# Kernel tuning notes

Hardware: AMD Instinct MI355X
Metric: run time of the kernel (lower is better)

The kernel has to match this reference:

```python
import jax, jax.numpy as jnp
import numpy as np

LEN = 8388608  # 2**23, must be a power of 2


def setup_inputs() -> dict:
    key = jax.random.key(0)
    k1, k2 = jax.random.split(key)
    inp = jax.random.normal(k1, (LEN,), dtype=jnp.float32)
    weight = jax.random.uniform(k2, (LEN // 2, 2), dtype=jnp.float32)  # learned twiddle factors
    return {"input": inp, "weight": weight}


def _complex_mul(a, w):
    # a: [d, cols, 2] complex pairs; w: [cols, 2] broadcast over leading dim
    ar, ai = a[:, :, 0], a[:, :, 1]
    wr, wi = w[:, 0], w[:, 1]
    return jnp.stack([ar * wr - ai * wi, ar * wi + ai * wr], axis=-1)


def reference(input, weight):
    n = input.shape[0]
    # real signal -> complex pairs, shape [n, 1, 2]
    x = jnp.stack([input, jnp.zeros_like(input)], axis=-1)[:, None, :]
    d = n // 2
    while d != 0:  # log2(n) static stages
        w = weight[0::d]          # [cols, 2] where cols == x.shape[1]
        top = x[:d]               # [d, cols, 2]
        bot = x[d:]               # [d, cols, 2]
        p = _complex_mul(bot, w)  # butterfly twiddle multiply
        x = jnp.concatenate([top + p, top - p], axis=1)  # [d, 2*cols, 2]
        d //= 2
    return x  # [1, n, 2]
```

## Files before the change

### kernel.cpp

```cpp
#include <hip/hip_runtime.h>
#include <hip/hip_fp16.h>

__device__ __forceinline__ float2 cadd(float2 a, float2 b) { return make_float2(a.x + b.x, a.y + b.y); }
__device__ __forceinline__ float2 csub(float2 a, float2 b) { return make_float2(a.x - b.x, a.y - b.y); }
__device__ __forceinline__ float2 cmul(float2 w, float2 z) {
    return make_float2(w.x * z.x - w.y * z.y, w.x * z.y + w.y * z.x);
}
__device__ __forceinline__ unsigned pk(float2 z) {
    __half2 h = __floats2half2_rn(z.x, z.y);
    return *reinterpret_cast<unsigned*>(&h);
}
__device__ __forceinline__ float2 upk(unsigned u) {
    __half2 h = *reinterpret_cast<__half2*>(&u);
    return __half22float2(h);
}

__host__ __device__ constexpr unsigned crev(unsigned x, int bits) {
    unsigned r = 0;
    for (int k = 0; k < bits; ++k) r |= ((x >> k) & 1u) << (bits - 1 - k);
    return r;
}


__global__ __launch_bounds__(256) void fft_pass_a(const float* __restrict__ in,
                                                  const float2* __restrict__ wt,
                                                  uint4* __restrict__ outp)
{
    __shared__ float2 L[4096];
    const int tid = threadIdx.x;
    const int l0  = blockIdx.x << 4;
    const int c   = tid & 15;
    const int qb  = tid >> 4;

    float2 pw1[4], pw2a[4], pw2b[4];
#pragma unroll
    for (int k = 0; k < 4; ++k) { pw1[k] = wt[0]; pw2a[k] = wt[0]; pw2b[k] = wt[1 << 21]; }

    {
        const int c4 = tid & 3, gg = tid >> 2;
#pragma unroll
        for (int k = 0; k < 4; ++k) {
            const int g = gg + (k << 6);
            const float4 v = *reinterpret_cast<const float4*>(in + ((size_t)g << 15) + l0 + (c4 << 2));
            const int base = (g << 4) + (c4 << 2);
            L[base + 0] = make_float2(v.x, 0.f);
            L[base + 1] = make_float2(v.y, 0.f);
            L[base + 2] = make_float2(v.z, 0.f);
            L[base + 3] = make_float2(v.w, 0.f);
        }
    }
    __syncthreads();

#pragma unroll
    for (int rho = 0; rho < 4; ++rho) {
        const int s = rho << 1, H = 128 >> s, Q = H >> 1, lo = 6 - s;
        float2 nw1[4], nw2a[4], nw2b[4];
        if (rho < 3) {
            const int s2 = s + 2, lo2 = 6 - s2;
#pragma unroll
            for (int k = 0; k < 4; ++k) {
                const int qi = (qb << 2) + k;
                const int b  = ((qi >> lo2) << (lo2 + 2)) | (qi & ((1 << lo2) - 1));
                const int jl = (int)(__brev((unsigned)(b >> (8 - s2))) >> (32 - s2));
                const int e  = jl << (21 - s2);
                nw1[k] = wt[e << 1]; nw2a[k] = wt[e]; nw2b[k] = wt[e + (1 << 21)];
            }
        }
#pragma unroll
        for (int k = 0; k < 4; ++k) {
            const int qi = (qb << 2) + k;
            const int b  = ((qi >> lo) << (lo + 2)) | (qi & ((1 << lo) - 1));
            const int iA = (b << 4) + c;
            const float2 A  = L[iA];
            const float2 Bv = L[iA + (Q << 4)];
            const float2 Cv = L[iA + (H << 4)];
            const float2 Dv = L[iA + ((H + Q) << 4)];
            const float2 pC = cmul(pw1[k], Cv), pD = cmul(pw1[k], Dv);
            const float2 tA = cadd(A, pC),  tC = csub(A, pC);
            const float2 tB = cadd(Bv, pD), tD = csub(Bv, pD);
            const float2 p2 = cmul(pw2a[k], tB);
            const float2 p3 = cmul(pw2b[k], tD);
            L[iA]                  = cadd(tA, p2);
            L[iA + (Q << 4)]       = csub(tA, p2);
            L[iA + (H << 4)]       = cadd(tC, p3);
            L[iA + ((H + Q) << 4)] = csub(tC, p3);
        }
        __syncthreads();
        if (rho < 3) {
#pragma unroll
            for (int k = 0; k < 4; ++k) { pw1[k] = nw1[k]; pw2a[k] = nw2a[k]; pw2b[k] = nw2b[k]; }
        }
    }

    {
        const int c4 = tid & 3, gg = tid >> 2;
#pragma unroll
        for (int k = 0; k < 4; ++k) {
            const int g  = gg + (k << 6);
            const int li = (g << 4) + (c4 << 2);
            uint4 v;
            v.x = pk(L[li]); v.y = pk(L[li + 1]); v.z = pk(L[li + 2]); v.w = pk(L[li + 3]);
            outp[((size_t)g << 13) + (l0 >> 2) + c4] = v;
        }
    }
}

__global__ __launch_bounds__(256) void fft_pass_b(const unsigned* __restrict__ in,
                                                  const float2* __restrict__ wt,
                                                  unsigned* __restrict__ out)
{
    const int tid = threadIdx.x;
    const int h   = blockIdx.x >> 2;
    const int low = ((blockIdx.x & 3) << 8) | tid;
    const unsigned hrev = __brev((unsigned)h) >> 24;
    const unsigned base = ((unsigned)h << 15) | (unsigned)low;

    float2 X[32];
#pragma unroll
    for (int m = 0; m < 32; ++m) X[m] = upk(in[base + ((unsigned)m << 10)]);

#pragma unroll
    for (int s = 0; s < 5; ++s) {
        const int half = 1 << (4 - s);
#pragma unroll
        for (int j = 0; j < 16; ++j) {
            const int mh = j >> (4 - s);
            const int lo = (mh << (5 - s)) | (j & (half - 1));
            const int hi = lo | half;
            const unsigned cr = crev((unsigned)mh, s);
            const float2 w = wt[(((cr << 8) | hrev) << (14 - s))];
            const float2 p = cmul(w, X[hi]);
            X[hi] = csub(X[lo], p);
            X[lo] = cadd(X[lo], p);
        }
    }
#pragma unroll
    for (int m = 0; m < 32; ++m) out[base + ((unsigned)m << 10)] = pk(X[m]);
}

__global__ __launch_bounds__(512, 4) void fft_pass_c(const uint4* __restrict__ inp4,
                                                     const float2* __restrict__ wt,
                                                     float2* __restrict__ out)
{
    extern __shared__ float2 L[];
    const int tid = threadIdx.x;
    const int h0  = blockIdx.x;
    const int lam = tid & 7;
    const int bq  = tid >> 3;
    const int R   = (h0 << 3) | lam;

    {
        const int f  = tid & 63;
        const int lm = tid >> 6;
        const unsigned H = __brev((unsigned)((h0 << 3) | lm)) >> 19;
        const size_t gb = ((size_t)H << 8);
#pragma unroll
        for (int k = 0; k < 4; ++k) {
            const uint4 v = inp4[gb + (k << 6) + f];
            const int base = lm * 1026 + (k << 8) + (f << 2);
            const float2 e0 = upk(v.x), e1 = upk(v.y), e2 = upk(v.z), e3 = upk(v.w);
            *reinterpret_cast<float4*>(&L[base])     = make_float4(e0.x, e0.y, e1.x, e1.y);
            *reinterpret_cast<float4*>(&L[base + 2]) = make_float4(e2.x, e2.y, e3.x, e3.y);
        }
    }
    __syncthreads();

#pragma unroll
    for (int rho = 0; rho < 4; ++rho) {
        const int sh = 8 - (rho << 1);
        const int Q  = 1 << sh;
        const int H2 = Q << 1;
#pragma unroll
        for (int k = 0; k < 4; ++k) {
            const int qi = (k << 6) | bq;
            const int x  = ((qi >> sh) << (sh + 2)) | (qi & (Q - 1));
            const int a  = x >> (sh + 2);
            const unsigned xr = rho ? (__brev((unsigned)a) >> (32 - (rho << 1))) : 0u;
            const int e  = (int)((((xr << 13) | (unsigned)R)) << sh);
            const float2 w1  = wt[e << 1];
            const float2 w2a = wt[e];
            const float2 w2b = wt[e + (1 << 21)];
            const int iA = lam * 1026 + x;
            const float2 A  = L[iA];
            const float2 Bv = L[iA + Q];
            const float2 Cv = L[iA + H2];
            const float2 Dv = L[iA + H2 + Q];
            const float2 pC = cmul(w1, Cv), pD = cmul(w1, Dv);
            const float2 tA = cadd(A, pC),  tC = csub(A, pC);
            const float2 tB = cadd(Bv, pD), tD = csub(Bv, pD);
            const float2 p2 = cmul(w2a, tB);
            const float2 p3 = cmul(w2b, tD);
            L[iA]           = cadd(tA, p2);
            L[iA + Q]       = csub(tA, p2);
            L[iA + H2]      = cadd(tC, p3);
            L[iA + H2 + Q]  = csub(tC, p3);
        }
        __syncthreads();
    }

    {
#pragma unroll
        for (int k = 0; k < 4; ++k) {
            const int qi = (k << 6) | bq;
            const int x  = qi << 2;
            const unsigned xr = __brev((unsigned)qi) >> 24;
            const int e  = (int)((xr << 13) | (unsigned)R);
            const float2 w1  = wt[e << 1];
            const float2 w2a = wt[e];
            const float2 w2b = wt[e + (1 << 21)];
            const int iA = lam * 1026 + x;
            const float4 f0 = *reinterpret_cast<const float4*>(&L[iA]);
            const float4 f1 = *reinterpret_cast<const float4*>(&L[iA + 2]);
            const float2 A  = make_float2(f0.x, f0.y);
            const float2 Bv = make_float2(f0.z, f0.w);
            const float2 Cv = make_float2(f1.x, f1.y);
            const float2 Dv = make_float2(f1.z, f1.w);
            const float2 pC = cmul(w1, Cv), pD = cmul(w1, Dv);
            const float2 tA = cadd(A, pC),  tC = csub(A, pC);
            const float2 tB = cadd(Bv, pD), tD = csub(Bv, pD);
            const float2 p2 = cmul(w2a, tB);
            const float2 p3 = cmul(w2b, tD);
            const float2 rA = cadd(tA, p2), rB = csub(tA, p2);
            const float2 rC = cadd(tC, p3), rD = csub(tC, p3);
            *reinterpret_cast<float4*>(&L[iA])     = make_float4(rA.x, rA.y, rB.x, rB.y);
            *reinterpret_cast<float4*>(&L[iA + 2]) = make_float4(rC.x, rC.y, rD.x, rD.y);
        }
    }
    __syncthreads();

    {
        const int l2 = (tid & 3) << 1;
        const int xb = tid >> 2;
#pragma unroll
        for (int k = 0; k < 8; ++k) {
            const int x = (k << 7) | xb;
            const float2 a0 = L[l2 * 1026 + x];
            const float2 a1 = L[(l2 + 1) * 1026 + x];
            const size_t o = ((size_t)(__brev((unsigned)x) >> 22) << 13)
                           | (unsigned)((h0 << 3) | l2);
            *reinterpret_cast<float4*>(out + o) = make_float4(a0.x, a0.y, a1.x, a1.y);
        }
    }
}

extern "C" void kernel_launch(void* const* d_in, const int* in_sizes, int n_in,
                              void* d_out, int out_size, void* d_ws, size_t ws_size,
                              hipStream_t stream)
{
    (void)in_sizes; (void)n_in; (void)out_size; (void)ws_size;
    const float*  in = (const float*)d_in[0];
    const float2* wt = (const float2*)d_in[1];
    float2* outc = (float2*)d_out;
    uint4*  buf1 = (uint4*)d_ws;
    unsigned* buf2 = (unsigned*)((char*)d_ws + (32u << 20));

    static bool attr_done = false;
    if (!attr_done) {
        (void)hipFuncSetAttribute(reinterpret_cast<const void*>(fft_pass_c),
                                  hipFuncAttributeMaxDynamicSharedMemorySize, 8 * 1026 * 8);
        attr_done = true;
    }

    fft_pass_a<<<2048, 256, 0, stream>>>(in, wt, buf1);
    fft_pass_b<<<1024, 256, 0, stream>>>((const unsigned*)buf1, wt, buf2);
    fft_pass_c<<<1024, 512, 8 * 1026 * 8, stream>>>((const uint4*)buf2, wt, outc);
}
```

Before: 198.4 us.

## Use nontemporal loads/stores, widen pass C blocks, prefetch twiddles, swizzle block order

Global loads and stores in all three passes become nontemporal so streaming data does not pollute the caches. Pass C now runs 1024 threads per block, with two butterflies per thread instead of four. Its twiddles are prefetched into registers one stage ahead so their latency overlaps the LDS work, and the block index is permuted to change which blocks run together. This trades more registers and higher occupancy pressure for better latency hiding, and the nontemporal hints could hurt if data would have been reused in L2.

Result: no change. 201.7 us (+1.7%).

```diff
diff --git a/kernel.cpp b/kernel.cpp
--- a/kernel.cpp
+++ b/kernel.cpp
@@ -1,5 +1,8 @@
 #include <hip/hip_runtime.h>
 #include <hip/hip_fp16.h>
+
+typedef float    f4 __attribute__((ext_vector_type(4)));
+typedef unsigned u4 __attribute__((ext_vector_type(4)));
 
 __device__ __forceinline__ float2 cadd(float2 a, float2 b) { return make_float2(a.x + b.x, a.y + b.y); }
 __device__ __forceinline__ float2 csub(float2 a, float2 b) { return make_float2(a.x - b.x, a.y - b.y); }
@@ -41,12 +44,13 @@
 #pragma unroll
         for (int k = 0; k < 4; ++k) {
             const int g = gg + (k << 6);
-            const float4 v = *reinterpret_cast<const float4*>(in + ((size_t)g << 15) + l0 + (c4 << 2));
+            const f4 v = __builtin_nontemporal_load(
+                reinterpret_cast<const f4*>(in + ((size_t)g << 15) + l0 + (c4 << 2)));
             const int base = (g << 4) + (c4 << 2);
-            L[base + 0] = make_float2(v.x, 0.f);
-            L[base + 1] = make_float2(v.y, 0.f);
-            L[base + 2] = make_float2(v.z, 0.f);
-            L[base + 3] = make_float2(v.w, 0.f);
+            L[base + 0] = make_float2(v[0], 0.f);
+            L[base + 1] = make_float2(v[1], 0.f);
+            L[base + 2] = make_float2(v[2], 0.f);
+            L[base + 3] = make_float2(v[3], 0.f);
         }
     }
     __syncthreads();
@@ -98,9 +102,10 @@
         for (int k = 0; k < 4; ++k) {
             const int g  = gg + (k << 6);
             const int li = (g << 4) + (c4 << 2);
-            uint4 v;
-            v.x = pk(L[li]); v.y = pk(L[li + 1]); v.z = pk(L[li + 2]); v.w = pk(L[li + 3]);
-            outp[((size_t)g << 13) + (l0 >> 2) + c4] = v;
+            u4 v;
+            v[0] = pk(L[li]); v[1] = pk(L[li + 1]); v[2] = pk(L[li + 2]); v[3] = pk(L[li + 3]);
+            __builtin_nontemporal_store(v,
+                reinterpret_cast<u4*>(&outp[((size_t)g << 13) + (l0 >> 2) + c4]));
         }
     }
 }
@@ -117,7 +122,8 @@
 
     float2 X[32];
 #pragma unroll
-    for (int m = 0; m < 32; ++m) X[m] = upk(in[base + ((unsigned)m << 10)]);
+    for (int m = 0; m < 32; ++m)
+        X[m] = upk(__builtin_nontemporal_load(&in[base + ((unsigned)m << 10)]));
 
 #pragma unroll
     for (int s = 0; s < 5; ++s) {
@@ -135,34 +141,47 @@
         }
     }
 #pragma unroll
-    for (int m = 0; m < 32; ++m) out[base + ((unsigned)m << 10)] = pk(X[m]);
-}
-
-__global__ __launch_bounds__(512, 4) void fft_pass_c(const uint4* __restrict__ inp4,
-                                                     const float2* __restrict__ wt,
-                                                     float2* __restrict__ out)
+    for (int m = 0; m < 32; ++m)
+        __builtin_nontemporal_store(pk(X[m]), &out[base + ((unsigned)m << 10)]);
+}
+
+__global__ __launch_bounds__(1024, 8) void fft_pass_c(const uint4* __restrict__ inp4,
+                                                      const float2* __restrict__ wt,
+                                                      float2* __restrict__ out)
 {
     extern __shared__ float2 L[];
     const int tid = threadIdx.x;
-    const int h0  = blockIdx.x;
+    const int bid = blockIdx.x;
+    const int h0  = ((bid & 7) << 7) | (bid >> 3);
     const int lam = tid & 7;
     const int bq  = tid >> 3;
     const int R   = (h0 << 3) | lam;
 
     {
-        const int f  = tid & 63;
-        const int lm = tid >> 6;
+        const int f    = tid & 63;
+        const int lm   = (tid >> 6) & 7;
+        const int half = tid >> 9;
         const unsigned H = __brev((unsigned)((h0 << 3) | lm)) >> 19;
         const size_t gb = ((size_t)H << 8);
 #pragma unroll
-        for (int k = 0; k < 4; ++k) {
-            const uint4 v = inp4[gb + (k << 6) + f];
-            const int base = lm * 1026 + (k << 8) + (f << 2);
-            const float2 e0 = upk(v.x), e1 = upk(v.y), e2 = upk(v.z), e3 = upk(v.w);
+        for (int k = 0; k < 2; ++k) {
+            const int slot = (half << 7) | (k << 6) | f;
+            const u4 v = __builtin_nontemporal_load(
+                reinterpret_cast<const u4*>(&inp4[gb + slot]));
+            const int base = lm * 1026 + (slot << 2);
+            const float2 e0 = upk(v[0]), e1 = upk(v[1]), e2 = upk(v[2]), e3 = upk(v[3]);
             *reinterpret_cast<float4*>(&L[base])     = make_float4(e0.x, e0.y, e1.x, e1.y);
             *reinterpret_cast<float4*>(&L[base + 2]) = make_float4(e2.x, e2.y, e3.x, e3.y);
         }
     }
+
+    float2 w1[2], w2a[2], w2b[2];
+#pragma unroll
+    for (int k = 0; k < 2; ++k) {
+        const int e = R << 8;
+        w1[k] = wt[e << 1]; w2a[k] = wt[e]; w2b[k] = wt[e + (1 << 21)];
+    }
+    float2 f1[2], f2a[2], f2b[2];
     __syncthreads();
 
 #pragma unroll
@@ -170,56 +189,69 @@
         const int sh = 8 - (rho << 1);
         const int Q  = 1 << sh;
         const int H2 = Q << 1;
-#pragma unroll
-        for (int k = 0; k < 4; ++k) {
-            const int qi = (k << 6) | bq;
+        float2 nw1[2], nw2a[2], nw2b[2];
+        if (rho < 3) {
+            const int rn = rho + 1, shn = 8 - (rn << 1);
+#pragma unroll
+            for (int k = 0; k < 2; ++k) {
+                const int qi = (k << 7) | bq;
+                const unsigned ar = (unsigned)(qi >> shn);
+                const unsigned xr = __brev(ar) >> (32 - (rn << 1));
+                const int e = (int)(((xr << 13) | (unsigned)R) << shn);
+                nw1[k] = wt[e << 1]; nw2a[k] = wt[e]; nw2b[k] = wt[e + (1 << 21)];
+            }
+        } else {
+#pragma unroll
+            for (int k = 0; k < 2; ++k) {
+                const int qi = (k << 7) | bq;
+                const unsigned xr = __brev((unsigned)qi) >> 24;
+                const int e = (int)((xr << 13) | (unsigned)R);
+                f1[k] = wt[e << 1]; f2a[k] = wt[e]; f2b[k] = wt[e + (1 << 21)];
+            }
+        }
+#pragma unroll
+        for (int k = 0; k < 2; ++k) {
+            const int qi = (k << 7) | bq;
             const int x  = ((qi >> sh) << (sh + 2)) | (qi & (Q - 1));
-            const int a  = x >> (sh + 2);
-            const unsigned xr = rho ? (__brev((unsigned)a) >> (32 - (rho << 1))) : 0u;
-            const int e  = (int)((((xr << 13) | (unsigned)R)) << sh);
-            const float2 w1  = wt[e << 1];
-            const float2 w2a = wt[e];
-            const float2 w2b = wt[e + (1 << 21)];
             const int iA = lam * 1026 + x;
             const float2 A  = L[iA];
             const float2 Bv = L[iA + Q];
             const float2 Cv = L[iA + H2];
             const float2 Dv = L[iA + H2 + Q];
-            const float2 pC = cmul(w1, Cv), pD = cmul(w1, Dv);
+            const float2 pC = cmul(w1[k], Cv), pD = cmul(w1[k], Dv);
             const float2 tA = cadd(A, pC),  tC = csub(A, pC);
             const float2 tB = cadd(Bv, pD), tD = csub(Bv, pD);
-            const float2 p2 = cmul(w2a, tB);
-            const float2 p3 = cmul(w2b, tD);
+            const float2 p2 = cmul(w2a[k], tB);
+            const float2 p3 = cmul(w2b[k], tD);
             L[iA]           = cadd(tA, p2);
             L[iA + Q]       = csub(tA, p2);
             L[iA + H2]      = cadd(tC, p3);
             L[iA + H2 + Q]  = csub(tC, p3);
         }
         __syncthreads();
-    }
-
-    {
-#pragma unroll
-        for (int k = 0; k < 4; ++k) {
-            const int qi = (k << 6) | bq;
+        if (rho < 3) {
+#pragma unroll
+            for (int k = 0; k < 2; ++k) { w1[k] = nw1[k]; w2a[k] = nw2a[k]; w2b[k] = nw2b[k]; }
+        }
+    }
+
+    {
+#pragma unroll
+        for (int k = 0; k < 2; ++k) {
+            const int qi = (k << 7) | bq;
             const int x  = qi << 2;
-            const unsigned xr = __brev((unsigned)qi) >> 24;
-            const int e  = (int)((xr << 13) | (unsigned)R);
-            const float2 w1  = wt[e << 1];
-            const float2 w2a = wt[e];
-            const float2 w2b = wt[e + (1 << 21)];
             const int iA = lam * 1026 + x;
-            const float4 f0 = *reinterpret_cast<const float4*>(&L[iA]);
-            const float4 f1 = *reinterpret_cast<const float4*>(&L[iA + 2]);
-            const float2 A  = make_float2(f0.x, f0.y);
-            const float2 Bv = make_float2(f0.z, f0.w);
-            const float2 Cv = make_float2(f1.x, f1.y);
-            const float2 Dv = make_float2(f1.z, f1.w);
-            const float2 pC = cmul(w1, Cv), pD = cmul(w1, Dv);
+            const float4 g0 = *reinterpret_cast<const float4*>(&L[iA]);
+            const float4 g1 = *reinterpret_cast<const float4*>(&L[iA + 2]);
+            const float2 A  = make_float2(g0.x, g0.y);
+            const float2 Bv = make_float2(g0.z, g0.w);
+            const float2 Cv = make_float2(g1.x, g1.y);
+            const float2 Dv = make_float2(g1.z, g1.w);
+            const float2 pC = cmul(f1[k], Cv), pD = cmul(f1[k], Dv);
             const float2 tA = cadd(A, pC),  tC = csub(A, pC);
             const float2 tB = cadd(Bv, pD), tD = csub(Bv, pD);
-            const float2 p2 = cmul(w2a, tB);
-            const float2 p3 = cmul(w2b, tD);
+            const float2 p2 = cmul(f2a[k], tB);
+            const float2 p3 = cmul(f2b[k], tD);
             const float2 rA = cadd(tA, p2), rB = csub(tA, p2);
             const float2 rC = cadd(tC, p3), rD = csub(tC, p3);
             *reinterpret_cast<float4*>(&L[iA])     = make_float4(rA.x, rA.y, rB.x, rB.y);
@@ -229,16 +261,17 @@
     __syncthreads();
 
     {
-        const int l2 = (tid & 3) << 1;
-        const int xb = tid >> 2;
-#pragma unroll
-        for (int k = 0; k < 8; ++k) {
-            const int x = (k << 7) | xb;
+        const int l2   = (tid & 3) << 1;
+        const int rest = tid >> 2;
+#pragma unroll
+        for (int k = 0; k < 4; ++k) {
+            const int x = (k << 8) | rest;
             const float2 a0 = L[l2 * 1026 + x];
             const float2 a1 = L[(l2 + 1) * 1026 + x];
             const size_t o = ((size_t)(__brev((unsigned)x) >> 22) << 13)
                            | (unsigned)((h0 << 3) | l2);
-            *reinterpret_cast<float4*>(out + o) = make_float4(a0.x, a0.y, a1.x, a1.y);
+            f4 sv; sv[0] = a0.x; sv[1] = a0.y; sv[2] = a1.x; sv[3] = a1.y;
+            __builtin_nontemporal_store(sv, reinterpret_cast<f4*>(out + o));
         }
     }
 }
@@ -263,5 +296,5 @@
 
     fft_pass_a<<<2048, 256, 0, stream>>>(in, wt, buf1);
     fft_pass_b<<<1024, 256, 0, stream>>>((const unsigned*)buf1, wt, buf2);
-    fft_pass_c<<<1024, 512, 8 * 1026 * 8, stream>>>((const uint4*)buf2, wt, outc);
-}
+    fft_pass_c<<<1024, 1024, 8 * 1026 * 8, stream>>>((const uint4*)buf2, wt, outc);
+}
```

## Merge three FFT passes into two kernels with 12+11 stage split

Applied to the files above, without the earlier changes.

Restructures the 23-stage FFT from three global-memory passes into two. The first kernel does 12 stages per column set using registers and a padded shared-memory transpose, and the second does the remaining 11 stages in shared memory. This removes one full round trip of the fp16 intermediate buffer through global memory. In exchange it uses larger blocks (1024 threads), more shared memory per block, and more register pressure, so occupancy may drop.

New measurement: 226.0 us. 1.14x slower.

```diff
diff --git a/kernel.cpp b/kernel.cpp
--- a/kernel.cpp
+++ b/kernel.cpp
@@ -14,6 +14,11 @@
     __half2 h = *reinterpret_cast<__half2*>(&u);
     return __half22float2(h);
 }
+__device__ __forceinline__ void bf(float2& lo, float2& hi, float2 w) {
+    const float2 p = cmul(w, hi);
+    hi = csub(lo, p);
+    lo = cadd(lo, p);
+}
 
 __host__ __device__ constexpr unsigned crev(unsigned x, int bits) {
     unsigned r = 0;
@@ -22,103 +27,24 @@
 }
 
 
-__global__ __launch_bounds__(256) void fft_pass_a(const float* __restrict__ in,
+__global__ __launch_bounds__(1024) void fft_pass1(const float* __restrict__ in,
                                                   const float2* __restrict__ wt,
-                                                  uint4* __restrict__ outp)
+                                                  unsigned* __restrict__ outp)
 {
-    __shared__ float2 L[4096];
-    const int tid = threadIdx.x;
-    const int l0  = blockIdx.x << 4;
-    const int c   = tid & 15;
-    const int qb  = tid >> 4;
-
-    float2 pw1[4], pw2a[4], pw2b[4];
-#pragma unroll
-    for (int k = 0; k < 4; ++k) { pw1[k] = wt[0]; pw2a[k] = wt[0]; pw2b[k] = wt[1 << 21]; }
-
+    extern __shared__ unsigned LD[];
+    const int tid  = threadIdx.x;
+    const int col0 = blockIdx.x << 3;
+    const int c    = tid & 7;
+
+    float2 X[32];
+
+    const int f = tid >> 3;
     {
-        const int c4 = tid & 3, gg = tid >> 2;
-#pragma unroll
-        for (int k = 0; k < 4; ++k) {
-            const int g = gg + (k << 6);
-            const float4 v = *reinterpret_cast<const float4*>(in + ((size_t)g << 15) + l0 + (c4 << 2));
-            const int base = (g << 4) + (c4 << 2);
-            L[base + 0] = make_float2(v.x, 0.f);
-            L[base + 1] = make_float2(v.y, 0.f);
-            L[base + 2] = make_float2(v.z, 0.f);
-            L[base + 3] = make_float2(v.w, 0.f);
-        }
-    }
-    __syncthreads();
-
-#pragma unroll
-    for (int rho = 0; rho < 4; ++rho) {
-        const int s = rho << 1, H = 128 >> s, Q = H >> 1, lo = 6 - s;
-        float2 nw1[4], nw2a[4], nw2b[4];
-        if (rho < 3) {
-            const int s2 = s + 2, lo2 = 6 - s2;
-#pragma unroll
-            for (int k = 0; k < 4; ++k) {
-                const int qi = (qb << 2) + k;
-                const int b  = ((qi >> lo2) << (lo2 + 2)) | (qi & ((1 << lo2) - 1));
-                const int jl = (int)(__brev((unsigned)(b >> (8 - s2))) >> (32 - s2));
-                const int e  = jl << (21 - s2);
-                nw1[k] = wt[e << 1]; nw2a[k] = wt[e]; nw2b[k] = wt[e + (1 << 21)];
-            }
-        }
-#pragma unroll
-        for (int k = 0; k < 4; ++k) {
-            const int qi = (qb << 2) + k;
-            const int b  = ((qi >> lo) << (lo + 2)) | (qi & ((1 << lo) - 1));
-            const int iA = (b << 4) + c;
-            const float2 A  = L[iA];
-            const float2 Bv = L[iA + (Q << 4)];
-            const float2 Cv = L[iA + (H << 4)];
-            const float2 Dv = L[iA + ((H + Q) << 4)];
-            const float2 pC = cmul(pw1[k], Cv), pD = cmul(pw1[k], Dv);
-            const float2 tA = cadd(A, pC),  tC = csub(A, pC);
-            const float2 tB = cadd(Bv, pD), tD = csub(Bv, pD);
-            const float2 p2 = cmul(pw2a[k], tB);
-            const float2 p3 = cmul(pw2b[k], tD);
-            L[iA]                  = cadd(tA, p2);
-            L[iA + (Q << 4)]       = csub(tA, p2);
-            L[iA + (H << 4)]       = cadd(tC, p3);
-            L[iA + ((H + Q) << 4)] = csub(tC, p3);
-        }
-        __syncthreads();
-        if (rho < 3) {
-#pragma unroll
-            for (int k = 0; k < 4; ++k) { pw1[k] = nw1[k]; pw2a[k] = nw2a[k]; pw2b[k] = nw2b[k]; }
-        }
-    }
-
-    {
-        const int c4 = tid & 3, gg = tid >> 2;
-#pragma unroll
-        for (int k = 0; k < 4; ++k) {
-            const int g  = gg + (k << 6);
-            const int li = (g << 4) + (c4 << 2);
-            uint4 v;
-            v.x = pk(L[li]); v.y = pk(L[li + 1]); v.z = pk(L[li + 2]); v.w = pk(L[li + 3]);
-            outp[((size_t)g << 13) + (l0 >> 2) + c4] = v;
-        }
-    }
-}
-
-__global__ __launch_bounds__(256) void fft_pass_b(const unsigned* __restrict__ in,
-                                                  const float2* __restrict__ wt,
-                                                  unsigned* __restrict__ out)
-{
-    const int tid = threadIdx.x;
-    const int h   = blockIdx.x >> 2;
-    const int low = ((blockIdx.x & 3) << 8) | tid;
-    const unsigned hrev = __brev((unsigned)h) >> 24;
-    const unsigned base = ((unsigned)h << 15) | (unsigned)low;
-
-    float2 X[32];
-#pragma unroll
-    for (int m = 0; m < 32; ++m) X[m] = upk(in[base + ((unsigned)m << 10)]);
-
+        const size_t base = ((size_t)f << 11) + (size_t)(col0 + c);
+#pragma unroll
+        for (int a = 0; a < 32; ++a)
+            X[a] = make_float2(in[base + ((size_t)a << 18)], 0.f);
+    }
 #pragma unroll
     for (int s = 0; s < 5; ++s) {
         const int half = 1 << (4 - s);
@@ -127,60 +53,111 @@
             const int mh = j >> (4 - s);
             const int lo = (mh << (5 - s)) | (j & (half - 1));
             const int hi = lo | half;
-            const unsigned cr = crev((unsigned)mh, s);
-            const float2 w = wt[(((cr << 8) | hrev) << (14 - s))];
-            const float2 p = cmul(w, X[hi]);
-            X[hi] = csub(X[lo], p);
-            X[lo] = cadd(X[lo], p);
-        }
-    }
-#pragma unroll
-    for (int m = 0; m < 32; ++m) out[base + ((unsigned)m << 10)] = pk(X[m]);
-}
-
-__global__ __launch_bounds__(512, 4) void fft_pass_c(const uint4* __restrict__ inp4,
-                                                     const float2* __restrict__ wt,
-                                                     float2* __restrict__ out)
+            bf(X[lo], X[hi], wt[crev((unsigned)mh, s) << (22 - s)]);
+        }
+    }
+#pragma unroll
+    for (int a = 0; a < 32; ++a)
+        LD[(((a << 7) | f) * 9) + c] = pk(X[a]);
+    __syncthreads();
+
+    const int at = tid >> 5;
+    const int d  = (tid >> 3) & 3;
+    const unsigned ra = __brev((unsigned)at) >> 27;
+#pragma unroll
+    for (int b = 0; b < 32; ++b)
+        X[b] = upk(LD[(((at << 7) | (b << 2) | d) * 9) + c]);
+#pragma unroll
+    for (int s = 0; s < 5; ++s) {
+        const int half = 1 << (4 - s);
+#pragma unroll
+        for (int j = 0; j < 16; ++j) {
+            const int mh = j >> (4 - s);
+            const int lo = (mh << (5 - s)) | (j & (half - 1));
+            const int hi = lo | half;
+            bf(X[lo], X[hi], wt[((crev((unsigned)mh, s) << 5) | ra) << (17 - s)]);
+        }
+    }
+#pragma unroll
+    for (int b = 0; b < 32; ++b)
+        LD[(((at << 7) | (b << 2) | d) * 9) + c] = pk(X[b]);
+    __syncthreads();
+
+    const int bl = (tid >> 3) & 3;
+#pragma unroll
+    for (int dd = 0; dd < 4; ++dd)
+#pragma unroll
+        for (int bh = 0; bh < 8; ++bh)
+            X[(dd << 3) | bh] = upk(LD[(((at << 7) | (bh << 4) | (bl << 2) | dd) * 9) + c]);
+#pragma unroll
+    for (int bh = 0; bh < 8; ++bh) {
+        const unsigned b5 = (unsigned)((bh << 2) | bl);
+        const float2 w = wt[(((__brev(b5) >> 27) << 5) | ra) << 12];
+        bf(X[bh],      X[16 + bh], w);
+        bf(X[8 + bh],  X[24 + bh], w);
+    }
+#pragma unroll
+    for (int d1 = 0; d1 < 2; ++d1)
+#pragma unroll
+        for (int bh = 0; bh < 8; ++bh) {
+            const unsigned b5 = (unsigned)((bh << 2) | bl);
+            const float2 w = wt[((((unsigned)d1) << 10) | ((__brev(b5) >> 27) << 5) | ra) << 11];
+            bf(X[(d1 << 4) | bh], X[(d1 << 4) | 8 | bh], w);
+        }
+#pragma unroll
+    for (int dd = 0; dd < 4; ++dd)
+#pragma unroll
+        for (int bh = 0; bh < 8; ++bh) {
+            const size_t G = (size_t)((at << 7) | (bh << 4) | (bl << 2) | dd);
+            outp[(G << 11) + (size_t)(col0 + c)] = pk(X[(dd << 3) | bh]);
+        }
+}
+
+__global__ __launch_bounds__(1024) void fft_pass2(const unsigned* __restrict__ inp,
+                                                  const float2* __restrict__ wt,
+                                                  float2* __restrict__ out)
 {
     extern __shared__ float2 L[];
     const int tid = threadIdx.x;
     const int h0  = blockIdx.x;
     const int lam = tid & 7;
     const int bq  = tid >> 3;
-    const int R   = (h0 << 3) | lam;
+    const unsigned rP = (unsigned)((h0 << 3) | lam);
 
     {
-        const int f  = tid & 63;
-        const int lm = tid >> 6;
-        const unsigned H = __brev((unsigned)((h0 << 3) | lm)) >> 19;
-        const size_t gb = ((size_t)H << 8);
+        const int cs = tid >> 7, fq = tid & 127;
+        const unsigned P = __brev((unsigned)((h0 << 3) | cs)) >> 20;
+        const uint4* in4 = reinterpret_cast<const uint4*>(inp);
+        const size_t gb = ((size_t)P << 9);
 #pragma unroll
         for (int k = 0; k < 4; ++k) {
-            const uint4 v = inp4[gb + (k << 6) + f];
-            const int base = lm * 1026 + (k << 8) + (f << 2);
-            const float2 e0 = upk(v.x), e1 = upk(v.y), e2 = upk(v.z), e3 = upk(v.w);
-            *reinterpret_cast<float4*>(&L[base])     = make_float4(e0.x, e0.y, e1.x, e1.y);
-            *reinterpret_cast<float4*>(&L[base + 2]) = make_float4(e2.x, e2.y, e3.x, e3.y);
-        }
-    }
-    __syncthreads();
-
-#pragma unroll
-    for (int rho = 0; rho < 4; ++rho) {
-        const int sh = 8 - (rho << 1);
+            const int slot = (k << 7) | fq;
+            const uint4 v = in4[gb + slot];
+            const int basei = cs * 2052 + (slot << 2);
+            L[basei]     = upk(v.x);
+            L[basei + 1] = upk(v.y);
+            L[basei + 2] = upk(v.z);
+            L[basei + 3] = upk(v.w);
+        }
+    }
+    __syncthreads();
+
+#pragma unroll
+    for (int rho = 0; rho < 5; ++rho) {
+        const int sh = 9 - (rho << 1);
         const int Q  = 1 << sh;
         const int H2 = Q << 1;
 #pragma unroll
         for (int k = 0; k < 4; ++k) {
-            const int qi = (k << 6) | bq;
+            const int qi = (k << 7) | bq;
             const int x  = ((qi >> sh) << (sh + 2)) | (qi & (Q - 1));
-            const int a  = x >> (sh + 2);
-            const unsigned xr = rho ? (__brev((unsigned)a) >> (32 - (rho << 1))) : 0u;
-            const int e  = (int)((((xr << 13) | (unsigned)R)) << sh);
+            const unsigned ar = (unsigned)(x >> (sh + 2));
+            const unsigned xr = rho ? (__brev(ar) >> (32 - (rho << 1))) : 0u;
+            const unsigned e  = ((xr << 12) | rP) << sh;
             const float2 w1  = wt[e << 1];
             const float2 w2a = wt[e];
-            const float2 w2b = wt[e + (1 << 21)];
-            const int iA = lam * 1026 + x;
+            const float2 w2b = wt[e + (1u << 21)];
+            const int iA = lam * 2052 + x;
             const float2 A  = L[iA];
             const float2 Bv = L[iA + Q];
             const float2 Cv = L[iA + H2];
@@ -198,33 +175,17 @@
         __syncthreads();
     }
 
-    {
-#pragma unroll
-        for (int k = 0; k < 4; ++k) {
-            const int qi = (k << 6) | bq;
-            const int x  = qi << 2;
-            const unsigned xr = __brev((unsigned)qi) >> 24;
-            const int e  = (int)((xr << 13) | (unsigned)R);
-            const float2 w1  = wt[e << 1];
-            const float2 w2a = wt[e];
-            const float2 w2b = wt[e + (1 << 21)];
-            const int iA = lam * 1026 + x;
-            const float4 f0 = *reinterpret_cast<const float4*>(&L[iA]);
-            const float4 f1 = *reinterpret_cast<const float4*>(&L[iA + 2]);
-            const float2 A  = make_float2(f0.x, f0.y);
-            const float2 Bv = make_float2(f0.z, f0.w);
-            const float2 Cv = make_float2(f1.x, f1.y);
-            const float2 Dv = make_float2(f1.z, f1.w);
-            const float2 pC = cmul(w1, Cv), pD = cmul(w1, Dv);
-            const float2 tA = cadd(A, pC),  tC = csub(A, pC);
-            const float2 tB = cadd(Bv, pD), tD = csub(Bv, pD);
-            const float2 p2 = cmul(w2a, tB);
-            const float2 p3 = cmul(w2b, tD);
-            const float2 rA = cadd(tA, p2), rB = csub(tA, p2);
-            const float2 rC = cadd(tC, p3), rD = csub(tC, p3);
-            *reinterpret_cast<float4*>(&L[iA])     = make_float4(rA.x, rA.y, rB.x, rB.y);
-            *reinterpret_cast<float4*>(&L[iA + 2]) = make_float4(rC.x, rC.y, rD.x, rD.y);
-        }
+#pragma unroll
+    for (int k = 0; k < 8; ++k) {
+        const int pq = (k << 7) | bq;
+        const int iA = lam * 2052 + (pq << 1);
+        const unsigned e = ((__brev((unsigned)pq) >> 22) << 12) | rP;
+        const float2 w = wt[e];
+        const float2 A  = L[iA];
+        const float2 Bv = L[iA + 1];
+        const float2 p  = cmul(w, Bv);
+        L[iA]     = cadd(A, p);
+        L[iA + 1] = csub(A, p);
     }
     __syncthreads();
 
@@ -233,11 +194,11 @@
         const int xb = tid >> 2;
 #pragma unroll
         for (int k = 0; k < 8; ++k) {
-            const int x = (k << 7) | xb;
-            const float2 a0 = L[l2 * 1026 + x];
-            const float2 a1 = L[(l2 + 1) * 1026 + x];
-            const size_t o = ((size_t)(__brev((unsigned)x) >> 22) << 13)
-                           | (unsigned)((h0 << 3) | l2);
+            const int x = (k << 8) | xb;
+            const unsigned rx = __brev((unsigned)x) >> 21;
+            const float2 a0 = L[l2 * 2052 + x];
+            const float2 a1 = L[(l2 + 1) * 2052 + x];
+            const size_t o = ((size_t)rx << 12) | (size_t)((h0 << 3) | l2);
             *reinterpret_cast<float4*>(out + o) = make_float4(a0.x, a0.y, a1.x, a1.y);
         }
     }
@@ -251,17 +212,17 @@
     const float*  in = (const float*)d_in[0];
     const float2* wt = (const float2*)d_in[1];
     float2* outc = (float2*)d_out;
-    uint4*  buf1 = (uint4*)d_ws;
-    unsigned* buf2 = (unsigned*)((char*)d_ws + (32u << 20));
+    unsigned* buf1 = (unsigned*)d_ws;
 
     static bool attr_done = false;
     if (!attr_done) {
-        (void)hipFuncSetAttribute(reinterpret_cast<const void*>(fft_pass_c),
-                                  hipFuncAttributeMaxDynamicSharedMemorySize, 8 * 1026 * 8);
+        (void)hipFuncSetAttribute(reinterpret_cast<const void*>(fft_pass1),
+                                  hipFuncAttributeMaxDynamicSharedMemorySize, 4096 * 9 * 4);
+        (void)hipFuncSetAttribute(reinterpret_cast<const void*>(fft_pass2),
+                                  hipFuncAttributeMaxDynamicSharedMemorySize, 8 * 2052 * 8);
         attr_done = true;
     }
 
-    fft_pass_a<<<2048, 256, 0, stream>>>(in, wt, buf1);
-    fft_pass_b<<<1024, 256, 0, stream>>>((const unsigned*)buf1, wt, buf2);
-    fft_pass_c<<<1024, 512, 8 * 1026 * 8, stream>>>((const uint4*)buf2, wt, outc);
-}
+    fft_pass1<<<256, 1024, 4096 * 9 * 4, stream>>>(in, wt, buf1);
+    fft_pass2<<<512, 1024, 8 * 2052 * 8, stream>>>(buf1, wt, outc);
+}
```
